# Kernel optimization log

Hardware: AMD Instinct MI355X
Metric: run time of the kernel (lower is better)

## Reference

```python
import math
import jax, jax.numpy as jnp
import numpy as np

D_MODEL = 1024
N_HEADS = 16
HEAD_DIM = D_MODEL // N_HEADS
ROPE_BASE = 10000.0
EPS = 1e-6


def rmsnorm(x, w, eps=EPS):
    # x: (..., head_dim); computed in fp32 like the torch code
    xf = x.astype(jnp.float32)
    rms = jax.lax.rsqrt(jnp.mean(xf * xf, axis=-1, keepdims=True) + eps)
    return (xf * rms).astype(x.dtype) * w


def apply_rope(x, cos, sin):
    # x: (B, H, T, head_dim); cos/sin: (T, head_dim/2)
    d2 = x.shape[-1] // 2
    x1, x2 = x[..., :d2], x[..., d2:]
    c = cos[None, None, :, :]
    s = sin[None, None, :, :]
    return jnp.concatenate([x1 * c - x2 * s, x2 * c + x1 * s], axis=-1)


def setup_inputs() -> dict:
    key = jax.random.key(0)
    ks = jax.random.split(key, 7)
    B, T = 2, 2048
    x = jax.random.normal(ks[0], (B, T, D_MODEL), dtype=jnp.float32)
    scale = 1.0 / math.sqrt(D_MODEL)
    Wq = jax.random.normal(ks[1], (D_MODEL, D_MODEL), dtype=jnp.float32) * scale
    Wk = jax.random.normal(ks[2], (D_MODEL, D_MODEL), dtype=jnp.float32) * scale
    Wv = jax.random.normal(ks[3], (D_MODEL, D_MODEL), dtype=jnp.float32) * scale
    Wo = jax.random.normal(ks[4], (D_MODEL, D_MODEL), dtype=jnp.float32) * scale
    q_norm_w = jnp.ones((HEAD_DIM,), dtype=jnp.float32)
    k_norm_w = jnp.ones((HEAD_DIM,), dtype=jnp.float32)
    return {"x": x, "Wq": Wq, "Wk": Wk, "Wv": Wv, "Wo": Wo,
            "q_norm_w": q_norm_w, "k_norm_w": k_norm_w}


def reference(x, Wq, Wk, Wv, Wo, q_norm_w, k_norm_w):
    B, T, d = x.shape
    H, hd = N_HEADS, HEAD_DIM
    # projections (nn.Linear applies x @ W.T; here W is stored as (in,out))
    q = (x @ Wq).reshape(B, T, H, hd).transpose(0, 2, 1, 3)  # (B,H,T,hd)
    k = (x @ Wk).reshape(B, T, H, hd).transpose(0, 2, 1, 3)
    v = (x @ Wv).reshape(B, T, H, hd).transpose(0, 2, 1, 3)
    # QK RMSNorm per head
    q = rmsnorm(q, q_norm_w)
    k = rmsnorm(k, k_norm_w)
    # rotary embeddings
    inv_freq = 1.0 / (ROPE_BASE ** (jnp.arange(0, hd, 2, dtype=jnp.float32) / hd))
    t = jnp.arange(T, dtype=jnp.float32)
    freqs = jnp.outer(t, inv_freq)  # (T, hd/2)
    cos, sin = jnp.cos(freqs), jnp.sin(freqs)
    q = apply_rope(q, cos, sin)
    k = apply_rope(k, cos, sin)
    # naive full attention with causal mask
    scale = 1.0 / math.sqrt(hd)
    attn = jnp.einsum('bhqd,bhkd->bhqk', q, k) * scale  # (B,H,T,T)
    causal = jnp.triu(jnp.full((T, T), -jnp.inf, dtype=attn.dtype), k=1)
    attn = attn + causal[None, None, :, :]
    attn = jax.nn.softmax(attn, axis=-1)
    out = jnp.einsum('bhqk,bhkd->bhqd', attn, v)
    out = out.transpose(0, 2, 1, 3).reshape(B, T, d)
    return out @ Wo
```

## Files before the change

### kernel.cpp

```cpp
#include <hip/hip_runtime.h>

typedef unsigned short u16;
typedef unsigned int   u32;
typedef __bf16 bf16x8 __attribute__((ext_vector_type(8)));
typedef float  f32x4  __attribute__((ext_vector_type(4)));
typedef float  f32x2  __attribute__((ext_vector_type(2)));
typedef u32    u32x4  __attribute__((ext_vector_type(4)));
typedef u16    u16x4  __attribute__((ext_vector_type(4)));

#define D_MODEL 1024
#define T_SEQ   2048
#define NH      16
#define HD      64

#define QSCALE  0.18033688011112042f
#define NEG8L2E -11.541560327111707f

__device__ __forceinline__ float b2f(u16 u){ return __uint_as_float(((u32)u)<<16); }
__device__ __forceinline__ u16 f2b(float f){
  u32 x = __float_as_uint(f);
  x += 0x7fffu + ((x>>16)&1u);
  return (u16)(x>>16);
}

__device__ __forceinline__ void gll16(const void* g, void* l){
  __builtin_amdgcn_global_load_lds((const __attribute__((address_space(1))) unsigned int*)g,
                                   (__attribute__((address_space(3))) unsigned int*)l, 16, 0, 0);
}

__global__ __launch_bounds__(256) void prep(
    const float* __restrict__ X, u16* __restrict__ Xb,
    const float* __restrict__ W0, const float* __restrict__ W1,
    const float* __restrict__ W2, const float* __restrict__ W3,
    u16* __restrict__ T0, u16* __restrict__ T1,
    u16* __restrict__ T2, u16* __restrict__ T3,
    float* __restrict__ cs)
{
  __shared__ u16 s[32][33];
  const int id = blockIdx.x, tid = threadIdx.x;
  if (id < 4096){
    const int i = (id*256 + tid)<<2;
    f32x4 v = *(const f32x4*)(X + i);
    u16x4 o;
    o[0]=f2b(v[0]); o[1]=f2b(v[1]); o[2]=f2b(v[2]); o[3]=f2b(v[3]);
    *(u16x4*)(Xb + i) = o;
  } else if (id < 8192){
    const int wid = id - 4096;
    const int z = wid >> 10, tile = wid & 1023;
    const float* src = (z==0)?W0:(z==1)?W1:(z==2)?W2:W3;
    u16*         dst = (z==0)?T0:(z==1)?T1:(z==2)?T2:T3;
    const int x = tid & 31, y = tid >> 5;
    const int r0 = (tile>>5)*32, c0 = (tile&31)*32;
    #pragma unroll
    for (int r=0;r<4;r++) s[y + r*8][x] = f2b(src[(r0 + y + r*8)*D_MODEL + c0 + x]);
    __syncthreads();
    #pragma unroll
    for (int r=0;r<4;r++) dst[(c0 + y + r*8)*D_MODEL + r0 + x] = s[x][y + r*8];
  } else {
    const int gid = (id-8192)*256 + tid;
    const int t = gid >> 5, fi = gid & 31;
    const float invf = expf(-(float)fi * 0.2878231366242558f);
    float sn, cn;
    sincosf((float)t * invf, &sn, &cn);
    cs[gid*2]   = cn;
    cs[gid*2+1] = sn;
  }
}

__global__ __launch_bounds__(256) void gemm_qkv(
    const u16* __restrict__ A, const u16* __restrict__ Bt,
    const float* __restrict__ qw, const float* __restrict__ kw,
    const float* __restrict__ cs,
    u16* __restrict__ Qb, u16* __restrict__ Kb, u16* __restrict__ Vt)
{
  __shared__ __align__(16) u16 sA[1024*8];
  __shared__ __align__(16) u16 sB[1024*8];
  const int id = blockIdx.x;
  const int xcd = id & 7, slot = id >> 3;
  const int bn = (xcd & 1)*12 + (slot % 12);
  const int bm = (xcd >> 1)*8 + (slot / 12);
  const int bm0 = bm<<7, bn0 = bn<<7;

  const int tid = threadIdx.x;
  const int lane = tid & 63;
  const int w  = tid>>6;
  const int wm = (w>>1)<<6;
  const int wn = (w&1)<<6;
  const int quad = lane>>4, lr = lane&15;
  const int swl = lr & 7;

  int rS[4], cS[4];
  #pragma unroll
  for (int i=0;i<4;i++){
    int s = i*256 + tid;
    rS[i] = s>>3;
    cS[i] = (s&7) ^ (rS[i]&7);
  }

  const f32x4 z4 = {0.f,0.f,0.f,0.f};
  f32x4 acc[4][4];
  #pragma unroll
  for (int i=0;i<4;i++)
    #pragma unroll
    for (int j=0;j<4;j++) acc[i][j] = z4;

  for (int kt=0; kt<D_MODEL; kt+=64){
    #pragma unroll
    for (int i=0;i<4;i++)
      gll16(A  + (bm0+rS[i])*D_MODEL + kt + cS[i]*8, sA + (i*256 + w*64)*8);
    #pragma unroll
    for (int i=0;i<4;i++)
      gll16(Bt + (bn0+rS[i])*D_MODEL + kt + cS[i]*8, sB + (i*256 + w*64)*8);
    __syncthreads();
    #pragma unroll
    for (int kk=0; kk<2; ++kk){
      bf16x8 af[4], bfr[4];
      const int cq = (kk*4 + quad) ^ swl;
      #pragma unroll
      for (int i=0;i<4;i++) af[i]  = *(const bf16x8*)(sA + ((wm + (i<<4) + lr)*8 + cq)*8);
      #pragma unroll
      for (int j=0;j<4;j++) bfr[j] = *(const bf16x8*)(sB + ((wn + (j<<4) + lr)*8 + cq)*8);
      #pragma unroll
      for (int i=0;i<4;i++)
        #pragma unroll
        for (int j=0;j<4;j++)
          acc[i][j] = __builtin_amdgcn_mfma_f32_16x16x32_bf16(af[i], bfr[j], acc[i][j], 0, 0, 0);
    }
    __syncthreads();
  }

  const int z = bn0 >> 10;
  const int ncl = bn0 & 1023;
  const int rq = quad<<2;

  if (z == 2){
    #pragma unroll
    for (int i=0;i<4;i++){
      int row0 = bm0 + wm + (i<<4) + rq;
      int bb = row0 >> 11, tt = row0 & (T_SEQ-1);
      #pragma unroll
      for (int j=0;j<4;j++){
        int nv = ncl + wn + (j<<4) + lr;
        int hh = nv >> 6, dd = nv & 63;
        u16* basep = Vt + ((bb*NH + hh)*HD + dd)*T_SEQ;
        #pragma unroll
        for (int r=0;r<4;r++){
          int t = tt + r;
          int pt = (t & ~63) + ((t&15)<<2) + ((t>>4)&3);
          basep[pt] = f2b(acc[i][j][r]);
        }
      }
    }
  } else {
    const float* w_ = (z==0) ? qw : kw;
    u16* dst = (z==0) ? Qb : Kb;
    const float scale = (z==0) ? QSCALE : 1.0f;
    float wv[4];
    #pragma unroll
    for (int j=0;j<4;j++) wv[j] = w_[(j<<4) + lr];
    #pragma unroll
    for (int i=0;i<4;i++){
      #pragma unroll
      for (int r=0;r<4;r++){
        const int grow = bm0 + wm + (i<<4) + rq + r;
        float ss = 0.f;
        #pragma unroll
        for (int j=0;j<4;j++) ss += acc[i][j][r]*acc[i][j][r];
        #pragma unroll
        for (int off=8; off>=1; off>>=1) ss += __shfl_xor(ss, off, 64);
        const float rms = rsqrtf(ss*(1.0f/64.0f) + 1e-6f);
        float xn[4];
        #pragma unroll
        for (int j=0;j<4;j++) xn[j] = acc[i][j][r]*rms*wv[j];
        const int t = grow & (T_SEQ-1);
        f32x2 c0 = *(const f32x2*)(cs + (t*32 + lr)*2);
        f32x2 c1 = *(const f32x2*)(cs + (t*32 + 16 + lr)*2);
        float o0 = xn[0]*c0[0] - xn[2]*c0[1];
        float o2 = xn[2]*c0[0] + xn[0]*c0[1];
        float o1 = xn[1]*c1[0] - xn[3]*c1[1];
        float o3 = xn[3]*c1[0] + xn[1]*c1[1];
        u16* rp = dst + grow*D_MODEL + ncl + wn + lr;
        rp[0]  = f2b(o0*scale);
        rp[16] = f2b(o1*scale);
        rp[32] = f2b(o2*scale);
        rp[48] = f2b(o3*scale);
      }
    }
  }
}

__global__ __launch_bounds__(256) void gemm_out(
    const u16* __restrict__ A, const u16* __restrict__ Bt, float* __restrict__ out)
{
  __shared__ __align__(16) u16 sA[1024*8];
  __shared__ __align__(16) u16 sB[1024*8];
  const int id = blockIdx.x;
  const int xcd = id & 7, slot = id >> 3;
  const int bn = slot & 7;
  const int bm = xcd*4 + (slot>>3);
  const int bm0 = bm<<7, bn0 = bn<<7;

  const int tid = threadIdx.x;
  const int lane = tid & 63;
  const int w  = tid>>6;
  const int wm = (w>>1)<<6;
  const int wn = (w&1)<<6;
  const int quad = lane>>4, lr = lane&15;
  const int swl = lr & 7;

  int rS[4], cS[4];
  #pragma unroll
  for (int i=0;i<4;i++){
    int s = i*256 + tid;
    rS[i] = s>>3;
    cS[i] = (s&7) ^ (rS[i]&7);
  }

  const f32x4 z4 = {0.f,0.f,0.f,0.f};
  f32x4 acc[4][4];
  #pragma unroll
  for (int i=0;i<4;i++)
    #pragma unroll
    for (int j=0;j<4;j++) acc[i][j] = z4;

  for (int kt=0; kt<D_MODEL; kt+=64){
    #pragma unroll
    for (int i=0;i<4;i++)
      gll16(A  + (bm0+rS[i])*D_MODEL + kt + cS[i]*8, sA + (i*256 + w*64)*8);
    #pragma unroll
    for (int i=0;i<4;i++)
      gll16(Bt + (bn0+rS[i])*D_MODEL + kt + cS[i]*8, sB + (i*256 + w*64)*8);
    __syncthreads();
    #pragma unroll
    for (int kk=0; kk<2; ++kk){
      bf16x8 af[4], bfr[4];
      const int cq = (kk*4 + quad) ^ swl;
      #pragma unroll
      for (int i=0;i<4;i++) af[i]  = *(const bf16x8*)(sA + ((wm + (i<<4) + lr)*8 + cq)*8);
      #pragma unroll
      for (int j=0;j<4;j++) bfr[j] = *(const bf16x8*)(sB + ((wn + (j<<4) + lr)*8 + cq)*8);
      #pragma unroll
      for (int i=0;i<4;i++)
        #pragma unroll
        for (int j=0;j<4;j++)
          acc[i][j] = __builtin_amdgcn_mfma_f32_16x16x32_bf16(af[i], bfr[j], acc[i][j], 0, 0, 0);
    }
    __syncthreads();
  }

  const int rq = quad<<2;
  #pragma unroll
  for (int i=0;i<4;i++){
    #pragma unroll
    for (int r=0;r<4;r++){
      const int grow = bm0 + wm + (i<<4) + rq + r;
      #pragma unroll
      for (int j=0;j<4;j++)
        out[grow*D_MODEL + bn0 + wn + (j<<4) + lr] = acc[i][j][r];
    }
  }
}

__global__ __launch_bounds__(256) void attn_mfma(const u16* __restrict__ Qb, const u16* __restrict__ Kb,
                                                 const u16* __restrict__ Vt, u16* __restrict__ AO)
{
  __shared__ __align__(16) u16 sK [2][4096];
  __shared__ __align__(16) u16 sVT[2][4096];
  __shared__ __align__(16) u16 sP [4][2048];
  const int tid = threadIdx.x;
  const int h  = blockIdx.x, b = blockIdx.y;
  const int zb = blockIdx.z;
  const int qt = (zb < 8) ? (15 - zb) : (zb - 8);
  const int w = tid>>6, lane = tid&63;
  const int quad = lane>>4, lr = lane&15;
  const int q8 = quad<<3;

  const int s0 = w*64 + lane, s1 = 256 + w*64 + lane;
  const int r0s = s0>>3, c0s = (s0&7)^(r0s&7);
  const int r1s = s1>>3, c1s = (s1&7)^(r1s&7);
  const u16* Kbase = Kb + (b*T_SEQ)*D_MODEL + h*HD;
  const u16* Vbase = Vt + (b*NH + h)*HD*T_SEQ;
  const int ldsOff0 = (w*64)*8, ldsOff1 = (256 + w*64)*8;

  bf16x8 qf[2][2];
  #pragma unroll
  for (int s=0;s<2;s++){
    const u16* Qrow = Qb + (b*T_SEQ + qt*128 + w*32 + s*16 + lr)*D_MODEL + h*HD;
    qf[s][0] = *(const bf16x8*)(Qrow + q8);
    qf[s][1] = *(const bf16x8*)(Qrow + 32 + q8);
  }

  f32x4 o[2][4];
  float lp[2][4];
  const f32x4 z4 = {0.f,0.f,0.f,0.f};
  const f32x4 ci = {NEG8L2E, NEG8L2E, NEG8L2E, NEG8L2E};
  #pragma unroll
  for (int s=0;s<2;s++)
    #pragma unroll
    for (int r=0;r<4;r++){ lp[s][r] = 0.f; }
  #pragma unroll
  for (int s=0;s<2;s++)
    #pragma unroll
    for (int nt=0;nt<4;nt++) o[s][nt] = z4;

  u16* myP = sP[w];
  const int nk = 2*qt + 2;

  gll16(Kbase + r0s*D_MODEL + c0s*8, &sK[0][ldsOff0]);
  gll16(Kbase + r1s*D_MODEL + c1s*8, &sK[0][ldsOff1]);
  gll16(Vbase + r0s*T_SEQ + c0s*8,   &sVT[0][ldsOff0]);
  gll16(Vbase + r1s*T_SEQ + c1s*8,   &sVT[0][ldsOff1]);
  __syncthreads();

  for (int kt=0; kt<nk; ++kt){
    const int cur = kt&1;
    if (kt+1 < nk){
      const int kn = kt+1, nb = cur^1;
      gll16(Kbase + (kn*64 + r0s)*D_MODEL + c0s*8, &sK[nb][ldsOff0]);
      gll16(Kbase + (kn*64 + r1s)*D_MODEL + c1s*8, &sK[nb][ldsOff1]);
      gll16(Vbase + r0s*T_SEQ + kn*64 + c0s*8,     &sVT[nb][ldsOff0]);
      gll16(Vbase + r1s*T_SEQ + kn*64 + c1s*8,     &sVT[nb][ldsOff1]);
    }

    f32x4 s4[2][4];
    #pragma unroll
    for (int ct=0; ct<4; ++ct){
      const int row = ct*16 + lr;
      const int sw = row&7;
      bf16x8 k0 = *(const bf16x8*)(&sK[cur][(row*8 + (quad     ^ sw))*8]);
      bf16x8 k1 = *(const bf16x8*)(&sK[cur][(row*8 + ((4+quad) ^ sw))*8]);
      #pragma unroll
      for (int s=0;s<2;s++){
        f32x4 acc = ci;
        acc = __builtin_amdgcn_mfma_f32_16x16x32_bf16(qf[s][0], k0, acc, 0,0,0);
        acc = __builtin_amdgcn_mfma_f32_16x16x32_bf16(qf[s][1], k1, acc, 0,0,0);
        s4[s][ct] = acc;
      }
    }

    if (kt >= nk-2){
      #pragma unroll
      for (int ct=0; ct<4; ++ct){
        const int colg = kt*64 + ct*16 + lr;
        #pragma unroll
        for (int s=0;s<2;s++){
          const int rowb = qt*128 + w*32 + s*16 + quad*4;
          #pragma unroll
          for (int r=0;r<4;r++)
            if (colg > rowb + r) s4[s][ct][r] = -1e30f;
        }
      }
    }

    #pragma unroll
    for (int s=0;s<2;s++){
      #pragma unroll
      for (int r=0;r<4;r++){
        u16x4 pk;
        #pragma unroll
        for (int ct=0; ct<4; ++ct){
          float p = exp2f(s4[s][ct][r]);
          u32 pu = __float_as_uint(p) & 0xffff0000u;
          lp[s][r] += __uint_as_float(pu);
          pk[ct] = (u16)(pu>>16);
        }
        const int prow = s*16 + quad*4 + r;
        const int pidx = prow*64 + (((lr>>1) ^ (prow&7))<<3) + ((lr&1)<<2);
        *(u16x4*)(myP + pidx) = pk;
      }
    }

    #pragma unroll
    for (int st=0; st<2; ++st){
      bf16x8 pf[2];
      #pragma unroll
      for (int s=0;s<2;s++){
        const int prow = s*16 + lr;
        pf[s] = *(const bf16x8*)(myP + prow*64 + (((st*4+quad) ^ (lr&7))<<3));
      }
      #pragma unroll
      for (int nt=0;nt<4;nt++){
        const int row = nt*16 + lr;
        const int slotv = row*8 + ((st*4+quad) ^ (row&7));
        bf16x8 vf = *(const bf16x8*)(&sVT[cur][slotv*8]);
        #pragma unroll
        for (int s=0;s<2;s++)
          o[s][nt] = __builtin_amdgcn_mfma_f32_16x16x32_bf16(pf[s], vf, o[s][nt], 0,0,0);
      }
    }
    __syncthreads();
  }

  #pragma unroll
  for (int s=0;s<2;s++)
    #pragma unroll
    for (int r=0;r<4;r++){
      #pragma unroll
      for (int off=8; off>=1; off>>=1) lp[s][r] += __shfl_xor(lp[s][r], off, 64);
    }
  #pragma unroll
  for (int s=0;s<2;s++){
    const int rowg = b*T_SEQ + qt*128 + w*32 + s*16 + quad*4;
    #pragma unroll
    for (int r=0;r<4;r++){
      float inv = 1.0f / lp[s][r];
      #pragma unroll
      for (int nt=0;nt<4;nt++)
        AO[(rowg + r)*D_MODEL + h*HD + nt*16 + lr] = f2b(o[s][nt][r]*inv);
    }
  }
}

extern "C" void kernel_launch(void* const* d_in, const int* in_sizes, int n_in,
                              void* d_out, int out_size, void* d_ws, size_t ws_size,
                              hipStream_t stream)
{
  const float* X  = (const float*)d_in[0];
  const float* Wq = (const float*)d_in[1];
  const float* Wk = (const float*)d_in[2];
  const float* Wv = (const float*)d_in[3];
  const float* Wo = (const float*)d_in[4];
  const float* qw = (const float*)d_in[5];
  const float* kw = (const float*)d_in[6];

  char* ws = (char*)d_ws;
  const size_t MB = 1024*1024;
  u16*   WqkvT = (u16*)(ws + 0*MB);
  u16*   WoT   = (u16*)(ws + 6*MB);
  u16*   Xb    = (u16*)(ws + 8*MB);
  u16*   Qb    = (u16*)(ws + 16*MB);
  u16*   Kb    = (u16*)(ws + 24*MB);
  u16*   Vt    = (u16*)(ws + 32*MB);
  u16*   AO    = (u16*)(ws + 40*MB);
  float* CS    = (float*)(ws + 48*MB);

  prep<<<dim3(8448), 256, 0, stream>>>(X, Xb, Wq, Wk, Wv, Wo,
      WqkvT, WqkvT + 1024*1024, WqkvT + 2*1024*1024, WoT, CS);
  gemm_qkv<<<dim3(768), 256, 0, stream>>>(Xb, WqkvT, qw, kw, CS, Qb, Kb, Vt);
  attn_mfma<<<dim3(NH, 2, 16), 256, 0, stream>>>(Qb, Kb, Vt, AO);
  gemm_out<<<dim3(256), 256, 0, stream>>>(AO, WoT, (float*)d_out);
}
```

Before: 209.3 us.

## Double-buffer QKV GEMM, shrink attention and out-proj tiles for more blocks

The QKV GEMM now uses a double-buffered LDS pipeline with K-step 32, prefetching the next tile while computing the current one. This replaces the single-buffer load-sync-compute pattern. Attention moves to 64-row query tiles with 128-thread blocks and twice as many blocks. The output GEMM uses 64x128 tiles with 512 blocks. Both of those raise parallelism and improve load balance across CUs, at the cost of less data reuse per block and more K/V reloads.

```diff
diff --git a/kernel.cpp b/kernel.cpp
--- a/kernel.cpp
+++ b/kernel.cpp
@@ -73,8 +73,8 @@
     const float* __restrict__ cs,
     u16* __restrict__ Qb, u16* __restrict__ Kb, u16* __restrict__ Vt)
 {
-  __shared__ __align__(16) u16 sA[1024*8];
-  __shared__ __align__(16) u16 sB[1024*8];
+  __shared__ __align__(16) u16 sA[2][512*8];
+  __shared__ __align__(16) u16 sB[2][512*8];
   const int id = blockIdx.x;
   const int xcd = id & 7, slot = id >> 3;
   const int bn = (xcd & 1)*12 + (slot % 12);
@@ -87,14 +87,15 @@
   const int wm = (w>>1)<<6;
   const int wn = (w&1)<<6;
   const int quad = lane>>4, lr = lane&15;
-  const int swl = lr & 7;
-
-  int rS[4], cS[4];
-  #pragma unroll
-  for (int i=0;i<4;i++){
+  const int cfr = (lr>>1)&3;
+
+  int rS[2], cS[2], lofs[2];
+  #pragma unroll
+  for (int i=0;i<2;i++){
     int s = i*256 + tid;
-    rS[i] = s>>3;
-    cS[i] = (s&7) ^ (rS[i]&7);
+    rS[i] = s>>2;
+    cS[i] = (s&3) ^ ((rS[i]>>1)&3);
+    lofs[i] = (i*256 + w*64)*8;
   }
 
   const f32x4 z4 = {0.f,0.f,0.f,0.f};
@@ -104,28 +105,34 @@
     #pragma unroll
     for (int j=0;j<4;j++) acc[i][j] = z4;
 
-  for (int kt=0; kt<D_MODEL; kt+=64){
+  #pragma unroll
+  for (int i=0;i<2;i++){
+    gll16(A  + (bm0+rS[i])*D_MODEL + cS[i]*8, &sA[0][lofs[i]]);
+    gll16(Bt + (bn0+rS[i])*D_MODEL + cS[i]*8, &sB[0][lofs[i]]);
+  }
+  __syncthreads();
+
+  for (int kt=0; kt<32; ++kt){
+    const int cur = kt&1;
+    if (kt < 31){
+      const int ko = (kt+1)*32, nb = cur^1;
+      #pragma unroll
+      for (int i=0;i<2;i++){
+        gll16(A  + (bm0+rS[i])*D_MODEL + ko + cS[i]*8, &sA[nb][lofs[i]]);
+        gll16(Bt + (bn0+rS[i])*D_MODEL + ko + cS[i]*8, &sB[nb][lofs[i]]);
+      }
+    }
+    bf16x8 af[4], bfr[4];
+    const int cq = (quad ^ cfr)<<3;
+    #pragma unroll
+    for (int i=0;i<4;i++) af[i]  = *(const bf16x8*)(&sA[cur][(wm + (i<<4) + lr)*32 + cq]);
+    #pragma unroll
+    for (int j=0;j<4;j++) bfr[j] = *(const bf16x8*)(&sB[cur][(wn + (j<<4) + lr)*32 + cq]);
     #pragma unroll
     for (int i=0;i<4;i++)
-      gll16(A  + (bm0+rS[i])*D_MODEL + kt + cS[i]*8, sA + (i*256 + w*64)*8);
-    #pragma unroll
-    for (int i=0;i<4;i++)
-      gll16(Bt + (bn0+rS[i])*D_MODEL + kt + cS[i]*8, sB + (i*256 + w*64)*8);
-    __syncthreads();
-    #pragma unroll
-    for (int kk=0; kk<2; ++kk){
-      bf16x8 af[4], bfr[4];
-      const int cq = (kk*4 + quad) ^ swl;
-      #pragma unroll
-      for (int i=0;i<4;i++) af[i]  = *(const bf16x8*)(sA + ((wm + (i<<4) + lr)*8 + cq)*8);
-      #pragma unroll
-      for (int j=0;j<4;j++) bfr[j] = *(const bf16x8*)(sB + ((wn + (j<<4) + lr)*8 + cq)*8);
-      #pragma unroll
-      for (int i=0;i<4;i++)
-        #pragma unroll
-        for (int j=0;j<4;j++)
-          acc[i][j] = __builtin_amdgcn_mfma_f32_16x16x32_bf16(af[i], bfr[j], acc[i][j], 0, 0, 0);
-    }
+      #pragma unroll
+      for (int j=0;j<4;j++)
+        acc[i][j] = __builtin_amdgcn_mfma_f32_16x16x32_bf16(af[i], bfr[j], acc[i][j], 0, 0, 0);
     __syncthreads();
   }
 
@@ -192,18 +199,18 @@
 __global__ __launch_bounds__(256) void gemm_out(
     const u16* __restrict__ A, const u16* __restrict__ Bt, float* __restrict__ out)
 {
-  __shared__ __align__(16) u16 sA[1024*8];
+  __shared__ __align__(16) u16 sA[512*8];
   __shared__ __align__(16) u16 sB[1024*8];
   const int id = blockIdx.x;
   const int xcd = id & 7, slot = id >> 3;
+  const int bm = xcd*8 + (slot>>3);
   const int bn = slot & 7;
-  const int bm = xcd*4 + (slot>>3);
-  const int bm0 = bm<<7, bn0 = bn<<7;
+  const int bm0 = bm<<6, bn0 = bn<<7;
 
   const int tid = threadIdx.x;
   const int lane = tid & 63;
   const int w  = tid>>6;
-  const int wm = (w>>1)<<6;
+  const int wm = (w>>1)<<5;
   const int wn = (w&1)<<6;
   const int quad = lane>>4, lr = lane&15;
   const int swl = lr & 7;
@@ -217,15 +224,15 @@
   }
 
   const f32x4 z4 = {0.f,0.f,0.f,0.f};
-  f32x4 acc[4][4];
-  #pragma unroll
-  for (int i=0;i<4;i++)
+  f32x4 acc[2][4];
+  #pragma unroll
+  for (int i=0;i<2;i++)
     #pragma unroll
     for (int j=0;j<4;j++) acc[i][j] = z4;
 
   for (int kt=0; kt<D_MODEL; kt+=64){
     #pragma unroll
-    for (int i=0;i<4;i++)
+    for (int i=0;i<2;i++)
       gll16(A  + (bm0+rS[i])*D_MODEL + kt + cS[i]*8, sA + (i*256 + w*64)*8);
     #pragma unroll
     for (int i=0;i<4;i++)
@@ -233,14 +240,14 @@
     __syncthreads();
     #pragma unroll
     for (int kk=0; kk<2; ++kk){
-      bf16x8 af[4], bfr[4];
+      bf16x8 af[2], bfr[4];
       const int cq = (kk*4 + quad) ^ swl;
       #pragma unroll
-      for (int i=0;i<4;i++) af[i]  = *(const bf16x8*)(sA + ((wm + (i<<4) + lr)*8 + cq)*8);
+      for (int i=0;i<2;i++) af[i]  = *(const bf16x8*)(sA + ((wm + (i<<4) + lr)*8 + cq)*8);
       #pragma unroll
       for (int j=0;j<4;j++) bfr[j] = *(const bf16x8*)(sB + ((wn + (j<<4) + lr)*8 + cq)*8);
       #pragma unroll
-      for (int i=0;i<4;i++)
+      for (int i=0;i<2;i++)
         #pragma unroll
         for (int j=0;j<4;j++)
           acc[i][j] = __builtin_amdgcn_mfma_f32_16x16x32_bf16(af[i], bfr[j], acc[i][j], 0, 0, 0);
@@ -250,7 +257,7 @@
 
   const int rq = quad<<2;
   #pragma unroll
-  for (int i=0;i<4;i++){
+  for (int i=0;i<2;i++){
     #pragma unroll
     for (int r=0;r<4;r++){
       const int grow = bm0 + wm + (i<<4) + rq + r;
@@ -261,31 +268,34 @@
   }
 }
 
-__global__ __launch_bounds__(256) void attn_mfma(const u16* __restrict__ Qb, const u16* __restrict__ Kb,
+__global__ __launch_bounds__(128) void attn_mfma(const u16* __restrict__ Qb, const u16* __restrict__ Kb,
                                                  const u16* __restrict__ Vt, u16* __restrict__ AO)
 {
   __shared__ __align__(16) u16 sK [2][4096];
   __shared__ __align__(16) u16 sVT[2][4096];
-  __shared__ __align__(16) u16 sP [4][2048];
+  __shared__ __align__(16) u16 sP [2][2048];
   const int tid = threadIdx.x;
   const int h  = blockIdx.x, b = blockIdx.y;
-  const int zb = blockIdx.z;
-  const int qt = (zb < 8) ? (15 - zb) : (zb - 8);
+  const int qt = 31 - blockIdx.z;
   const int w = tid>>6, lane = tid&63;
   const int quad = lane>>4, lr = lane&15;
   const int q8 = quad<<3;
 
-  const int s0 = w*64 + lane, s1 = 256 + w*64 + lane;
-  const int r0s = s0>>3, c0s = (s0&7)^(r0s&7);
-  const int r1s = s1>>3, c1s = (s1&7)^(r1s&7);
+  int rs[4], cs_[4], lof[4];
+  #pragma unroll
+  for (int i=0;i<4;i++){
+    int s = i*128 + tid;
+    rs[i] = s>>3;
+    cs_[i] = (s&7) ^ (rs[i]&7);
+    lof[i] = (i*128 + w*64)*8;
+  }
   const u16* Kbase = Kb + (b*T_SEQ)*D_MODEL + h*HD;
   const u16* Vbase = Vt + (b*NH + h)*HD*T_SEQ;
-  const int ldsOff0 = (w*64)*8, ldsOff1 = (256 + w*64)*8;
 
   bf16x8 qf[2][2];
   #pragma unroll
   for (int s=0;s<2;s++){
-    const u16* Qrow = Qb + (b*T_SEQ + qt*128 + w*32 + s*16 + lr)*D_MODEL + h*HD;
+    const u16* Qrow = Qb + (b*T_SEQ + qt*64 + w*32 + s*16 + lr)*D_MODEL + h*HD;
     qf[s][0] = *(const bf16x8*)(Qrow + q8);
     qf[s][1] = *(const bf16x8*)(Qrow + 32 + q8);
   }
@@ -297,29 +307,30 @@
   #pragma unroll
   for (int s=0;s<2;s++)
     #pragma unroll
-    for (int r=0;r<4;r++){ lp[s][r] = 0.f; }
+    for (int r=0;r<4;r++) lp[s][r] = 0.f;
   #pragma unroll
   for (int s=0;s<2;s++)
     #pragma unroll
     for (int nt=0;nt<4;nt++) o[s][nt] = z4;
 
   u16* myP = sP[w];
-  const int nk = 2*qt + 2;
-
-  gll16(Kbase + r0s*D_MODEL + c0s*8, &sK[0][ldsOff0]);
-  gll16(Kbase + r1s*D_MODEL + c1s*8, &sK[0][ldsOff1]);
-  gll16(Vbase + r0s*T_SEQ + c0s*8,   &sVT[0][ldsOff0]);
-  gll16(Vbase + r1s*T_SEQ + c1s*8,   &sVT[0][ldsOff1]);
+
+  #pragma unroll
+  for (int i=0;i<4;i++){
+    gll16(Kbase + rs[i]*D_MODEL + cs_[i]*8, &sK[0][lof[i]]);
+    gll16(Vbase + rs[i]*T_SEQ  + cs_[i]*8, &sVT[0][lof[i]]);
+  }
   __syncthreads();
 
-  for (int kt=0; kt<nk; ++kt){
+  for (int kt=0; kt<=qt; ++kt){
     const int cur = kt&1;
-    if (kt+1 < nk){
+    if (kt < qt){
       const int kn = kt+1, nb = cur^1;
-      gll16(Kbase + (kn*64 + r0s)*D_MODEL + c0s*8, &sK[nb][ldsOff0]);
-      gll16(Kbase + (kn*64 + r1s)*D_MODEL + c1s*8, &sK[nb][ldsOff1]);
-      gll16(Vbase + r0s*T_SEQ + kn*64 + c0s*8,     &sVT[nb][ldsOff0]);
-      gll16(Vbase + r1s*T_SEQ + kn*64 + c1s*8,     &sVT[nb][ldsOff1]);
+      #pragma unroll
+      for (int i=0;i<4;i++){
+        gll16(Kbase + (kn*64 + rs[i])*D_MODEL + cs_[i]*8, &sK[nb][lof[i]]);
+        gll16(Vbase + rs[i]*T_SEQ + kn*64 + cs_[i]*8,     &sVT[nb][lof[i]]);
+      }
     }
 
     f32x4 s4[2][4];
@@ -338,16 +349,16 @@
       }
     }
 
-    if (kt >= nk-2){
+    if (kt == qt){
       #pragma unroll
       for (int ct=0; ct<4; ++ct){
-        const int colg = kt*64 + ct*16 + lr;
+        int col = ct*16 + lr;
         #pragma unroll
         for (int s=0;s<2;s++){
-          const int rowb = qt*128 + w*32 + s*16 + quad*4;
+          const int rowb = w*32 + s*16 + quad*4;
           #pragma unroll
           for (int r=0;r<4;r++)
-            if (colg > rowb + r) s4[s][ct][r] = -1e30f;
+            if (col > rowb + r) s4[s][ct][r] = -1e30f;
         }
       }
     }
@@ -376,7 +387,7 @@
       #pragma unroll
       for (int s=0;s<2;s++){
         const int prow = s*16 + lr;
-        pf[s] = *(const bf16x8*)(myP + prow*64 + (((st*4+quad) ^ (lr&7))<<3));
+        pf[s] = *(const bf16x8*)(myP + prow*64 + (((st*4+quad) ^ (prow&7))<<3));
       }
       #pragma unroll
       for (int nt=0;nt<4;nt++){
@@ -400,7 +411,7 @@
     }
   #pragma unroll
   for (int s=0;s<2;s++){
-    const int rowg = b*T_SEQ + qt*128 + w*32 + s*16 + quad*4;
+    const int rowg = b*T_SEQ + qt*64 + w*32 + s*16 + quad*4;
     #pragma unroll
     for (int r=0;r<4;r++){
       float inv = 1.0f / lp[s][r];
@@ -437,6 +448,6 @@
   prep<<<dim3(8448), 256, 0, stream>>>(X, Xb, Wq, Wk, Wv, Wo,
       WqkvT, WqkvT + 1024*1024, WqkvT + 2*1024*1024, WoT, CS);
   gemm_qkv<<<dim3(768), 256, 0, stream>>>(Xb, WqkvT, qw, kw, CS, Qb, Kb, Vt);
-  attn_mfma<<<dim3(NH, 2, 16), 256, 0, stream>>>(Qb, Kb, Vt, AO);
-  gemm_out<<<dim3(256), 256, 0, stream>>>(AO, WoT, (float*)d_out);
-}
+  attn_mfma<<<dim3(NH, 2, 32), 128, 0, stream>>>(Qb, Kb, Vt, AO);
+  gemm_out<<<dim3(512), 256, 0, stream>>>(AO, WoT, (float*)d_out);
+}
```

After: 213.0 us. No clear change (+1.8%).
